# Performance work log

Hardware: AMD Instinct MI355X
Metric: run time of the kernel (lower is better)

The kernel has to match this reference:

```python
import jax, jax.numpy as jnp
import numpy as np

T, B, OBS, H, A = 512, 512, 128, 128, 18


def setup_inputs() -> dict:
    key = jax.random.key(0)
    ks = jax.random.split(key, 8)
    return {
        "hidden": jnp.zeros((B, H), jnp.float32),
        "obs": jax.random.normal(ks[0], (T, B, OBS), jnp.float32),
        "dones": jax.random.bernoulli(ks[1], 0.01, (T, B)),
        # embedding Dense (orthogonal-ish scale sqrt(2))
        "W_emb": jax.random.normal(ks[2], (OBS, H), jnp.float32) * (np.sqrt(2.0) / np.sqrt(OBS)).astype(np.float32),
        "b_emb": jnp.zeros((H,), jnp.float32),
        # GRUCell params: input path Wi/bi cover gates [r | z | n]; hidden path Wh (no bias for r,z), bhn for n
        "Wi": jax.random.normal(ks[3], (H, 3 * H), jnp.float32) / np.float32(np.sqrt(H)),
        "bi": jnp.zeros((3 * H,), jnp.float32),
        "Wh": jax.random.normal(ks[4], (H, 3 * H), jnp.float32) / np.float32(np.sqrt(H)),
        "bhn": jnp.zeros((H,), jnp.float32),
        # output Dense to action_dim
        "W_out": jax.random.normal(ks[5], (H, A), jnp.float32) / np.float32(np.sqrt(H)),
        "b_out": jnp.zeros((A,), jnp.float32),
    }


def reference(hidden, obs, dones, W_emb, b_emb, Wi, bi, Wh, bhn, W_out, b_out):
    # Dense embed + relu: [T, B, OBS] -> [T, B, H]
    emb = jax.nn.relu(obs @ W_emb + b_emb)
    # precompute input-path gate pre-activations for all steps: [T, B, 3H]
    gi = emb @ Wi + bi

    def step(h, xs):
        gi_t, reset = xs  # [B, 3H], [B]
        # reset-masked carry: initialize_carry gives zeros
        h = jnp.where(reset[:, None], jnp.zeros_like(h), h)
        gh = h @ Wh  # [B, 3H]
        r = jax.nn.sigmoid(gi_t[:, :H] + gh[:, :H])
        z = jax.nn.sigmoid(gi_t[:, H:2 * H] + gh[:, H:2 * H])
        n = jnp.tanh(gi_t[:, 2 * H:] + r * (gh[:, 2 * H:] + bhn))
        h_new = (1.0 - z) * n + z * h
        return h_new, h_new

    h_final, ys = jax.lax.scan(step, hidden, (gi, dones))  # ys: [T, B, H]
    q_vals = ys @ W_out + b_out  # [T, B, A]
    return (h_final, q_vals)
```

## Files before the change

### kernel.cpp

```cpp
#include <hip/hip_runtime.h>

#define T_DIM 512
#define B_DIM 512
#define OBS_DIM 128
#define H_DIM 128
#define A_DIM 18
#define G3 384
#define LDSS 136

#define SC_R (-1.44269504088896f)
#define SC_N (2.88539008177793f)

typedef _Float16 v8h __attribute__((ext_vector_type(8)));
typedef _Float16 v4h __attribute__((ext_vector_type(4)));
typedef float v4f __attribute__((ext_vector_type(4)));

#define EXP2F(x) __builtin_amdgcn_exp2f(x)
#define RCPF(x)  __builtin_amdgcn_rcpf(x)

#define BAR() asm volatile("s_waitcnt lgkmcnt(0)\n\ts_barrier" ::: "memory")

__global__ __launch_bounds__(512) void k1_embed_gi(
    const float* __restrict__ obs,
    const float* __restrict__ W_emb,
    const float* __restrict__ b_emb,
    const float* __restrict__ Wi,
    const float* __restrict__ bi,
    _Float16* __restrict__ gRZ,
    _Float16* __restrict__ gN)
{
    __shared__ __align__(16) _Float16 obs_lds[64 * LDSS];
    __shared__ __align__(16) _Float16 emb_lds[64 * LDSS];
    const int tid  = threadIdx.x;
    const int cg   = tid >> 6;
    const int lane = tid & 63;
    const int n16  = lane & 15;
    const int quad = lane >> 4;

    v8h fe[4];
    v8h fi[3][4];
#pragma unroll
    for (int kt = 0; kt < 4; ++kt)
#pragma unroll
        for (int j = 0; j < 8; ++j) {
            const int k = kt * 32 + quad * 8 + j;
            fe[kt][j] = (_Float16)W_emb[k * H_DIM + cg * 16 + n16];
        }
#pragma unroll
    for (int g = 0; g < 3; ++g) {
        const float sc = (g == 2) ? SC_N : SC_R;
#pragma unroll
        for (int kt = 0; kt < 4; ++kt)
#pragma unroll
            for (int j = 0; j < 8; ++j) {
                const int k = kt * 32 + quad * 8 + j;
                fi[g][kt][j] = (_Float16)(Wi[k * G3 + g * H_DIM + cg * 16 + n16] * sc);
            }
    }
    float bemb[4], bir[4], biz[4], bin_[4];
#pragma unroll
    for (int r = 0; r < 4; ++r) {
        const int col = cg * 16 + quad * 4 + r;
        bemb[r] = b_emb[col];
        bir[r]  = bi[col] * SC_R;
        biz[r]  = bi[H_DIM + col] * SC_R;
        bin_[r] = bi[2 * H_DIM + col] * SC_N;
    }

    const int srow = tid >> 3;
    const int sk   = (tid & 7) * 16;
    const int base = blockIdx.x * 16;

    {
        const float* op = obs + (size_t)(base * 64 + srow) * OBS_DIM + sk;
#pragma unroll
        for (int q = 0; q < 4; ++q) {
            const float4 a = *(const float4*)(op + q * 4);
            v4h pa = { (_Float16)a.x, (_Float16)a.y, (_Float16)a.z, (_Float16)a.w };
            *(v4h*)&obs_lds[srow * LDSS + sk + q * 4] = pa;
        }
    }
    __syncthreads();

    for (int i = 0; i < 16; ++i) {
        const int row0 = (base + i) * 64;
        const int ni = (i + 1 < 16) ? i + 1 : i;
        const float* opn = obs + (size_t)((base + ni) * 64 + srow) * OBS_DIM + sk;
        float4 nv[4];
#pragma unroll
        for (int q = 0; q < 4; ++q) nv[q] = *(const float4*)(opn + q * 4);

#pragma unroll
        for (int rt = 0; rt < 4; ++rt) {
            v8h bo[4];
#pragma unroll
            for (int kt = 0; kt < 4; ++kt)
                bo[kt] = *(const v8h*)&obs_lds[(rt * 16 + n16) * LDSS + kt * 32 + quad * 8];
            v4f ea = {0.f, 0.f, 0.f, 0.f};
#pragma unroll
            for (int kt = 0; kt < 4; ++kt)
                ea = __builtin_amdgcn_mfma_f32_16x16x32_f16(fe[kt], bo[kt], ea, 0, 0, 0);
            v4h e;
#pragma unroll
            for (int r = 0; r < 4; ++r) e[r] = (_Float16)fmaxf(ea[r] + bemb[r], 0.f);
            *(v4h*)&emb_lds[(rt * 16 + n16) * LDSS + cg * 16 + quad * 4] = e;
        }
        BAR();
#pragma unroll
        for (int rt = 0; rt < 4; ++rt) {
            v8h be[4];
#pragma unroll
            for (int kt = 0; kt < 4; ++kt)
                be[kt] = *(const v8h*)&emb_lds[(rt * 16 + n16) * LDSS + kt * 32 + quad * 8];
            v4f ar = {0.f,0.f,0.f,0.f}, az = {0.f,0.f,0.f,0.f}, an = {0.f,0.f,0.f,0.f};
#pragma unroll
            for (int kt = 0; kt < 4; ++kt) {
                ar = __builtin_amdgcn_mfma_f32_16x16x32_f16(fi[0][kt], be[kt], ar, 0, 0, 0);
                az = __builtin_amdgcn_mfma_f32_16x16x32_f16(fi[1][kt], be[kt], az, 0, 0, 0);
                an = __builtin_amdgcn_mfma_f32_16x16x32_f16(fi[2][kt], be[kt], an, 0, 0, 0);
            }
            const int R = row0 + rt * 16 + n16;
            v8h rz;
#pragma unroll
            for (int r = 0; r < 4; ++r) {
                rz[r]     = (_Float16)(ar[r] + bir[r]);
                rz[4 + r] = (_Float16)(az[r] + biz[r]);
            }
            *(v8h*)&gRZ[(size_t)R * 256 + cg * 32 + quad * 8] = rz;
            v4h nn;
#pragma unroll
            for (int r = 0; r < 4; ++r) nn[r] = (_Float16)(an[r] + bin_[r]);
            *(v4h*)&gN[(size_t)R * 128 + cg * 16 + quad * 4] = nn;
        }
#pragma unroll
        for (int q = 0; q < 4; ++q) {
            v4h pa = { (_Float16)nv[q].x, (_Float16)nv[q].y, (_Float16)nv[q].z, (_Float16)nv[q].w };
            *(v4h*)&obs_lds[srow * LDSS + sk + q * 4] = pa;
        }
        BAR();
    }
}

__global__ __launch_bounds__(512) void k2_recurrence(
    const float* __restrict__ hidden,
    const unsigned char* __restrict__ dones_raw,
    const _Float16* __restrict__ gRZ,
    _Float16* __restrict__ gN,
    const float* __restrict__ Wh,
    const float* __restrict__ bhn,
    float* __restrict__ out)
{
    __shared__ __align__(16) _Float16 h_lds[2][16 * LDSS];
    __shared__ __align__(16) unsigned char d_lds[(T_DIM + 1) * 16];
    __shared__ int byte_mode;
    const int tid  = threadIdx.x;
    const int w    = tid >> 6;
    const int lane = tid & 63;
    const int n16  = lane & 15;
    const int quad = lane >> 4;
    const int c16  = w * 16 + quad * 4;
    const int B0   = blockIdx.x * 16;

    if (tid == 0) byte_mode = 0;
    __syncthreads();
    {
        int hit = 0;
        for (int i = tid; i < 4096; i += 512)
            if ((i & 3) != 0 && dones_raw[i] == 1) hit = 1;
        if (hit) byte_mode = 1;
    }
    __syncthreads();
    const bool bm = (byte_mode != 0);

    {
        if (bm) {
            const int4 v = *(const int4*)(dones_raw + (size_t)tid * B_DIM + B0);
            *(int4*)&d_lds[tid * 16] = v;
        } else {
            const int* di = (const int*)dones_raw;
            const int* pp = di + (size_t)tid * B_DIM + B0;
            int4 wv; unsigned char* wb = (unsigned char*)&wv;
#pragma unroll
            for (int j = 0; j < 16; ++j) wb[j] = (unsigned char)(pp[j] != 0);
            *(int4*)&d_lds[tid * 16] = wv;
        }
        if (tid == 0) { int4 z = {0,0,0,0}; *(int4*)&d_lds[T_DIM * 16] = z; }
    }

    v8h fh[3][4];
#pragma unroll
    for (int g = 0; g < 3; ++g) {
        const float sc = (g == 2) ? SC_N : SC_R;
#pragma unroll
        for (int kt = 0; kt < 4; ++kt)
#pragma unroll
            for (int j = 0; j < 8; ++j) {
                const int k = kt * 32 + quad * 8 + j;
                fh[g][kt][j] = (_Float16)(Wh[k * G3 + g * H_DIM + w * 16 + n16] * sc);
            }
    }
    float bhnr[4];
#pragma unroll
    for (int r = 0; r < 4; ++r) bhnr[r] = bhn[c16 + r] * SC_N;

    __syncthreads();

    const bool d0 = d_lds[n16] != 0;
    float hu[4];
#pragma unroll
    for (int r = 0; r < 4; ++r) {
        const float hv = hidden[(size_t)(B0 + n16) * H_DIM + c16 + r];
        hu[r] = d0 ? 0.f : hv;
    }
    {
        v4h hw = { (_Float16)hu[0], (_Float16)hu[1], (_Float16)hu[2], (_Float16)hu[3] };
        *(v4h*)&h_lds[0][n16 * LDSS + c16] = hw;
    }

    const size_t RZT = (size_t)B_DIM * 256;
    const size_t NT  = (size_t)B_DIM * 128;
    const _Float16* rzp = gRZ + (size_t)(B0 + n16) * 256 + w * 32 + quad * 8;
    _Float16*       np  = gN  + (size_t)(B0 + n16) * 128 + c16;

    v8h s8_0 = *(const v8h*)(rzp);
    v4h s4_0 = *(const v4h*)(np);
    v8h s8_1 = *(const v8h*)(rzp + RZT);
    v4h s4_1 = *(const v4h*)(np + NT);
    const _Float16* pf8 = rzp + 2 * RZT;
    const _Float16* pf4 = np + 2 * NT;
    _Float16* yp = np;
    const unsigned char* dp = &d_lds[16 + n16];
    __syncthreads();

    auto STEP = [&](int t, v8h& s8, v4h& s4, const _Float16* hin, _Float16* hout)
        __attribute__((always_inline)) -> void {
        const v8h gC8 = *(const v8h*)pf8;
        const v4h gC4 = *(const v4h*)pf4;
        const unsigned char dnx = *dp;

        v8h bh[4];
#pragma unroll
        for (int kt = 0; kt < 4; ++kt)
            bh[kt] = *(const v8h*)&hin[n16 * LDSS + kt * 32 + quad * 8];

        v4f ga0 = {0.f,0.f,0.f,0.f}, ga1 = {0.f,0.f,0.f,0.f}, ga2 = {0.f,0.f,0.f,0.f};
#pragma unroll
        for (int kt = 0; kt < 4; ++kt) {
            ga0 = __builtin_amdgcn_mfma_f32_16x16x32_f16(fh[0][kt], bh[kt], ga0, 0, 0, 0);
            ga1 = __builtin_amdgcn_mfma_f32_16x16x32_f16(fh[1][kt], bh[kt], ga1, 0, 0, 0);
            ga2 = __builtin_amdgcn_mfma_f32_16x16x32_f16(fh[2][kt], bh[kt], ga2, 0, 0, 0);
        }

        float hn[4];
#pragma unroll
        for (int r = 0; r < 4; ++r) {
            const float er = EXP2F((float)s8[r] + ga0[r]);
            const float rg = RCPF(1.f + er);
            const float sn = fmaf(rg, ga2[r] + bhnr[r], (float)s4[r]);
            const float en = EXP2F(sn);
            const float ez = EXP2F((float)s8[4 + r] + ga1[r]);
            const float enp = en + 1.f;
            const float num = fmaf(hu[r], enp, (en - 1.f) * ez);
            const float den = enp * (1.f + ez);
            hn[r] = num * RCPF(den);
        }

        v4h yv = { (_Float16)hn[0], (_Float16)hn[1], (_Float16)hn[2], (_Float16)hn[3] };
        *(v4h*)yp = yv;

        const bool dn = dnx != 0;
        v4h hz = { (_Float16)0.f, (_Float16)0.f, (_Float16)0.f, (_Float16)0.f };
        v4h hv = dn ? hz : yv;
#pragma unroll
        for (int r = 0; r < 4; ++r) hu[r] = dn ? 0.f : hn[r];
        *(v4h*)&hout[n16 * LDSS + c16] = hv;

        s8 = gC8; s4 = gC4;
        const size_t adv = (t < 509) ? 1 : 0;
        pf8 += adv * RZT; pf4 += adv * NT;
        yp += NT; dp += 16;
        BAR();
    };

    for (int t = 0; t < T_DIM; t += 2) {
        STEP(t,     s8_0, s4_0, h_lds[0], h_lds[1]);
        STEP(t + 1, s8_1, s4_1, h_lds[1], h_lds[0]);
    }

#pragma unroll
    for (int r = 0; r < 4; ++r)
        out[(size_t)(B0 + n16) * H_DIM + c16 + r] = hu[r];
}

__global__ __launch_bounds__(256) void k3_qout(
    const _Float16* __restrict__ ys,
    const float* __restrict__ W_out,
    const float* __restrict__ b_out,
    float* __restrict__ qout)
{
    const int tid  = threadIdx.x;
    const int wv   = tid >> 6;
    const int lane = tid & 63;
    const int n16  = lane & 15;
    const int quad = lane >> 4;
    const int R0   = blockIdx.x * 64 + wv * 16;

    v8h fo[2][4];
#pragma unroll
    for (int ct = 0; ct < 2; ++ct)
#pragma unroll
        for (int kt = 0; kt < 4; ++kt)
#pragma unroll
            for (int j = 0; j < 8; ++j) {
                const int k = kt * 32 + quad * 8 + j;
                const int col = ct * 16 + n16;
                fo[ct][kt][j] = (col < A_DIM) ? (_Float16)W_out[k * A_DIM + col] : (_Float16)0.f;
            }
    float bq0[4], bq1[4];
#pragma unroll
    for (int r = 0; r < 4; ++r) {
        const int c0 = quad * 4 + r;
        const int c1 = 16 + quad * 4 + r;
        bq0[r] = b_out[c0];
        bq1[r] = (c1 < A_DIM) ? b_out[c1] : 0.f;
    }

    v8h by[4];
#pragma unroll
    for (int kt = 0; kt < 4; ++kt)
        by[kt] = *(const v8h*)(ys + (size_t)(R0 + n16) * 128 + kt * 32 + quad * 8);
    v4f q0 = {0.f,0.f,0.f,0.f}, q1 = {0.f,0.f,0.f,0.f};
#pragma unroll
    for (int kt = 0; kt < 4; ++kt) {
        q0 = __builtin_amdgcn_mfma_f32_16x16x32_f16(fo[0][kt], by[kt], q0, 0, 0, 0);
        q1 = __builtin_amdgcn_mfma_f32_16x16x32_f16(fo[1][kt], by[kt], q1, 0, 0, 0);
    }
    float* qp = qout + (size_t)(R0 + n16) * A_DIM;
#pragma unroll
    for (int r = 0; r < 4; ++r) qp[quad * 4 + r] = q0[r] + bq0[r];
    if (quad == 0) {
#pragma unroll
        for (int r = 0; r < 2; ++r) qp[16 + r] = q1[r] + bq1[r];
    }
}

extern "C" void kernel_launch(void* const* d_in, const int* in_sizes, int n_in,
                              void* d_out, int out_size, void* d_ws, size_t ws_size,
                              hipStream_t stream) {
    const float* hidden = (const float*)d_in[0];
    const float* obs    = (const float*)d_in[1];
    const unsigned char* dones = (const unsigned char*)d_in[2];
    const float* W_emb  = (const float*)d_in[3];
    const float* b_emb  = (const float*)d_in[4];
    const float* Wi     = (const float*)d_in[5];
    const float* bi     = (const float*)d_in[6];
    const float* Wh     = (const float*)d_in[7];
    const float* bhn    = (const float*)d_in[8];
    const float* W_out  = (const float*)d_in[9];
    const float* b_out  = (const float*)d_in[10];
    float* out = (float*)d_out;

    _Float16* gRZ = (_Float16*)d_ws;
    _Float16* gN  = gRZ + (size_t)T_DIM * B_DIM * 256;

    hipLaunchKernelGGL(k1_embed_gi, dim3(256), dim3(512), 0, stream,
                       obs, W_emb, b_emb, Wi, bi, gRZ, gN);
    hipLaunchKernelGGL(k2_recurrence, dim3(32), dim3(512), 0, stream,
                       hidden, dones, gRZ, gN, Wh, bhn, out);
    hipLaunchKernelGGL(k3_qout, dim3(4096), dim3(256), 0, stream,
                       gN, W_out, b_out, out + (size_t)B_DIM * H_DIM);
}
```

Baseline: 698.9 us.

## Process two 16-row batch tiles per recurrence block, halving grid size

The GRU recurrence kernel now has each block handle 32 batch rows as two 16-row tiles instead of 16, so the Wh fragments held in registers are reused across two MFMA chains per step. The grid drops from 32 to 16 blocks. The aim is to give each wave independent MFMA and transcendental work to overlap within the serial per-step chain, and to pay one barrier per step for twice as many rows. It also folds bhn into the n-gate accumulator init and switches to byte-offset addressing. The cost is more register pressure, a longer critical path per step, and only 16 CUs in use.

New measurement: 1.021 ms. +46.1%, slower.

```diff
diff --git a/kernel.cpp b/kernel.cpp
--- a/kernel.cpp
+++ b/kernel.cpp
@@ -150,8 +150,8 @@
     const float* __restrict__ bhn,
     float* __restrict__ out)
 {
-    __shared__ __align__(16) _Float16 h_lds[2][16 * LDSS];
-    __shared__ __align__(16) unsigned char d_lds[(T_DIM + 1) * 16];
+    __shared__ __align__(16) _Float16 h_lds[2][32 * LDSS];
+    __shared__ __align__(16) unsigned char d_lds[(T_DIM + 1) * 32];
     __shared__ int byte_mode;
     const int tid  = threadIdx.x;
     const int w    = tid >> 6;
@@ -159,7 +159,7 @@
     const int n16  = lane & 15;
     const int quad = lane >> 4;
     const int c16  = w * 16 + quad * 4;
-    const int B0   = blockIdx.x * 16;
+    const int B0   = blockIdx.x * 32;
 
     if (tid == 0) byte_mode = 0;
     __syncthreads();
@@ -173,18 +173,20 @@
     const bool bm = (byte_mode != 0);
 
     {
-        if (bm) {
-            const int4 v = *(const int4*)(dones_raw + (size_t)tid * B_DIM + B0);
-            *(int4*)&d_lds[tid * 16] = v;
-        } else {
-            const int* di = (const int*)dones_raw;
-            const int* pp = di + (size_t)tid * B_DIM + B0;
-            int4 wv; unsigned char* wb = (unsigned char*)&wv;
-#pragma unroll
-            for (int j = 0; j < 16; ++j) wb[j] = (unsigned char)(pp[j] != 0);
-            *(int4*)&d_lds[tid * 16] = wv;
-        }
-        if (tid == 0) { int4 z = {0,0,0,0}; *(int4*)&d_lds[T_DIM * 16] = z; }
+        for (int i = tid; i < T_DIM * 2; i += 512) {
+            const int t = i >> 1, half = i & 1;
+            if (bm) {
+                const int4 v = *(const int4*)(dones_raw + (size_t)t * B_DIM + B0 + half * 16);
+                *(int4*)&d_lds[t * 32 + half * 16] = v;
+            } else {
+                const int* pp = (const int*)dones_raw + (size_t)t * B_DIM + B0 + half * 16;
+                int4 wv; unsigned char* wb = (unsigned char*)&wv;
+#pragma unroll
+                for (int j = 0; j < 16; ++j) wb[j] = (unsigned char)(pp[j] != 0);
+                *(int4*)&d_lds[t * 32 + half * 16] = wv;
+            }
+        }
+        if (tid < 2) { int4 z = {0,0,0,0}; *(int4*)&d_lds[T_DIM * 32 + tid * 16] = z; }
     }
 
     v8h fh[3][4];
@@ -199,86 +201,115 @@
                 fh[g][kt][j] = (_Float16)(Wh[k * G3 + g * H_DIM + w * 16 + n16] * sc);
             }
     }
-    float bhnr[4];
-#pragma unroll
-    for (int r = 0; r < 4; ++r) bhnr[r] = bhn[c16 + r] * SC_N;
+    const v4f bhn_c = { bhn[c16] * SC_N, bhn[c16 + 1] * SC_N,
+                        bhn[c16 + 2] * SC_N, bhn[c16 + 3] * SC_N };
 
     __syncthreads();
 
-    const bool d0 = d_lds[n16] != 0;
-    float hu[4];
-#pragma unroll
-    for (int r = 0; r < 4; ++r) {
-        const float hv = hidden[(size_t)(B0 + n16) * H_DIM + c16 + r];
-        hu[r] = d0 ? 0.f : hv;
-    }
-    {
-        v4h hw = { (_Float16)hu[0], (_Float16)hu[1], (_Float16)hu[2], (_Float16)hu[3] };
-        *(v4h*)&h_lds[0][n16 * LDSS + c16] = hw;
-    }
-
-    const size_t RZT = (size_t)B_DIM * 256;
-    const size_t NT  = (size_t)B_DIM * 128;
-    const _Float16* rzp = gRZ + (size_t)(B0 + n16) * 256 + w * 32 + quad * 8;
-    _Float16*       np  = gN  + (size_t)(B0 + n16) * 128 + c16;
-
-    v8h s8_0 = *(const v8h*)(rzp);
-    v4h s4_0 = *(const v4h*)(np);
-    v8h s8_1 = *(const v8h*)(rzp + RZT);
-    v4h s4_1 = *(const v4h*)(np + NT);
-    const _Float16* pf8 = rzp + 2 * RZT;
-    const _Float16* pf4 = np + 2 * NT;
-    _Float16* yp = np;
-    const unsigned char* dp = &d_lds[16 + n16];
+    float hu[2][4];
+#pragma unroll
+    for (int rt = 0; rt < 2; ++rt) {
+        const bool d0 = d_lds[rt * 16 + n16] != 0;
+#pragma unroll
+        for (int r = 0; r < 4; ++r) {
+            const float hv = hidden[(size_t)(B0 + rt * 16 + n16) * H_DIM + c16 + r];
+            hu[rt][r] = d0 ? 0.f : hv;
+        }
+        v4h hw = { (_Float16)hu[rt][0], (_Float16)hu[rt][1],
+                   (_Float16)hu[rt][2], (_Float16)hu[rt][3] };
+        *(v4h*)&h_lds[0][(rt * 16 + n16) * LDSS + c16] = hw;
+    }
+
+    const int RZB = B_DIM * 256 * 2;
+    const int NB  = B_DIM * 128 * 2;
+    int rzo[2], no_[2];
+#pragma unroll
+    for (int rt = 0; rt < 2; ++rt) {
+        rzo[rt] = ((B0 + rt * 16 + n16) * 256 + w * 32 + quad * 8) * 2;
+        no_[rt] = ((B0 + rt * 16 + n16) * 128 + c16) * 2;
+    }
+    const char* gRZc = (const char*)gRZ;
+    char*       gNc  = (char*)gN;
+
+    v8h s8_0[2], s8_1[2]; v4h s4_0[2], s4_1[2];
+#pragma unroll
+    for (int rt = 0; rt < 2; ++rt) {
+        s8_0[rt] = *(const v8h*)(gRZc + rzo[rt]);
+        s8_1[rt] = *(const v8h*)(gRZc + RZB + rzo[rt]);
+        s4_0[rt] = *(const v4h*)(gNc + no_[rt]);
+        s4_1[rt] = *(const v4h*)(gNc + NB + no_[rt]);
+    }
+    const char* rzb = gRZc + (size_t)2 * RZB;
+    const char* nb  = gNc  + (size_t)2 * NB;
+    char*       yb  = gNc;
+    int dpo = 32 + n16;
     __syncthreads();
 
-    auto STEP = [&](int t, v8h& s8, v4h& s4, const _Float16* hin, _Float16* hout)
+    auto STEP = [&](int t, v8h (&s8)[2], v4h (&s4)[2],
+                    const _Float16* __restrict__ hin, _Float16* __restrict__ hout)
         __attribute__((always_inline)) -> void {
-        const v8h gC8 = *(const v8h*)pf8;
-        const v4h gC4 = *(const v4h*)pf4;
-        const unsigned char dnx = *dp;
-
-        v8h bh[4];
-#pragma unroll
-        for (int kt = 0; kt < 4; ++kt)
-            bh[kt] = *(const v8h*)&hin[n16 * LDSS + kt * 32 + quad * 8];
-
-        v4f ga0 = {0.f,0.f,0.f,0.f}, ga1 = {0.f,0.f,0.f,0.f}, ga2 = {0.f,0.f,0.f,0.f};
-#pragma unroll
-        for (int kt = 0; kt < 4; ++kt) {
-            ga0 = __builtin_amdgcn_mfma_f32_16x16x32_f16(fh[0][kt], bh[kt], ga0, 0, 0, 0);
-            ga1 = __builtin_amdgcn_mfma_f32_16x16x32_f16(fh[1][kt], bh[kt], ga1, 0, 0, 0);
-            ga2 = __builtin_amdgcn_mfma_f32_16x16x32_f16(fh[2][kt], bh[kt], ga2, 0, 0, 0);
-        }
-
-        float hn[4];
-#pragma unroll
-        for (int r = 0; r < 4; ++r) {
-            const float er = EXP2F((float)s8[r] + ga0[r]);
-            const float rg = RCPF(1.f + er);
-            const float sn = fmaf(rg, ga2[r] + bhnr[r], (float)s4[r]);
-            const float en = EXP2F(sn);
-            const float ez = EXP2F((float)s8[4 + r] + ga1[r]);
-            const float enp = en + 1.f;
-            const float num = fmaf(hu[r], enp, (en - 1.f) * ez);
-            const float den = enp * (1.f + ez);
-            hn[r] = num * RCPF(den);
-        }
-
-        v4h yv = { (_Float16)hn[0], (_Float16)hn[1], (_Float16)hn[2], (_Float16)hn[3] };
-        *(v4h*)yp = yv;
-
-        const bool dn = dnx != 0;
-        v4h hz = { (_Float16)0.f, (_Float16)0.f, (_Float16)0.f, (_Float16)0.f };
-        v4h hv = dn ? hz : yv;
-#pragma unroll
-        for (int r = 0; r < 4; ++r) hu[r] = dn ? 0.f : hn[r];
-        *(v4h*)&hout[n16 * LDSS + c16] = hv;
-
-        s8 = gC8; s4 = gC4;
-        const size_t adv = (t < 509) ? 1 : 0;
-        pf8 += adv * RZT; pf4 += adv * NT;
-        yp += NT; dp += 16;
+        v8h gC8[2]; v4h gC4[2]; unsigned char dnx[2];
+#pragma unroll
+        for (int rt = 0; rt < 2; ++rt) gC8[rt] = *(const v8h*)(rzb + rzo[rt]);
+#pragma unroll
+        for (int rt = 0; rt < 2; ++rt) gC4[rt] = *(const v4h*)(nb + no_[rt]);
+#pragma unroll
+        for (int rt = 0; rt < 2; ++rt) dnx[rt] = d_lds[dpo + rt * 16];
+
+        v8h bh[2][4];
+#pragma unroll
+        for (int rt = 0; rt < 2; ++rt)
+#pragma unroll
+            for (int kt = 0; kt < 4; ++kt)
+                bh[rt][kt] = *(const v8h*)&hin[(rt * 16 + n16) * LDSS + kt * 32 + quad * 8];
+
+        v4f ga0[2], ga1[2], ga2[2];
+#pragma unroll
+        for (int rt = 0; rt < 2; ++rt) {
+            ga0[rt] = (v4f){0.f,0.f,0.f,0.f};
+            ga1[rt] = (v4f){0.f,0.f,0.f,0.f};
+            ga2[rt] = bhn_c;
+        }
+#pragma unroll
+        for (int rt = 0; rt < 2; ++rt)
+#pragma unroll
+            for (int kt = 0; kt < 4; ++kt) {
+                ga0[rt] = __builtin_amdgcn_mfma_f32_16x16x32_f16(fh[0][kt], bh[rt][kt], ga0[rt], 0, 0, 0);
+                ga1[rt] = __builtin_amdgcn_mfma_f32_16x16x32_f16(fh[1][kt], bh[rt][kt], ga1[rt], 0, 0, 0);
+                ga2[rt] = __builtin_amdgcn_mfma_f32_16x16x32_f16(fh[2][kt], bh[rt][kt], ga2[rt], 0, 0, 0);
+            }
+
+#pragma unroll
+        for (int rt = 0; rt < 2; ++rt) {
+            float hn[4];
+#pragma unroll
+            for (int r = 0; r < 4; ++r) {
+                const float er  = EXP2F((float)s8[rt][r] + ga0[rt][r]);
+                const float rg  = RCPF(1.f + er);
+                const float sn  = fmaf(rg, ga2[rt][r], (float)s4[rt][r]);
+                const float en  = EXP2F(sn);
+                const float ez  = EXP2F((float)s8[rt][4 + r] + ga1[rt][r]);
+                const float enp = en + 1.f;
+                const float num = fmaf(hu[rt][r], enp, (en - 1.f) * ez);
+                const float den = enp * (1.f + ez);
+                hn[r] = num * RCPF(den);
+            }
+
+            v4h yv = { (_Float16)hn[0], (_Float16)hn[1], (_Float16)hn[2], (_Float16)hn[3] };
+            *(v4h*)(yb + no_[rt]) = yv;
+
+            const bool dn = dnx[rt] != 0;
+            v4h hz = { (_Float16)0.f, (_Float16)0.f, (_Float16)0.f, (_Float16)0.f };
+            v4h hv = dn ? hz : yv;
+#pragma unroll
+            for (int r = 0; r < 4; ++r) hu[rt][r] = dn ? 0.f : hn[r];
+            *(v4h*)&hout[(rt * 16 + n16) * LDSS + c16] = hv;
+
+            s8[rt] = gC8[rt]; s4[rt] = gC4[rt];
+        }
+
+        if (t <= 508) { rzb += RZB; nb += NB; }
+        yb += NB; dpo += 32;
         BAR();
     };
 
@@ -288,8 +319,10 @@
     }
 
 #pragma unroll
-    for (int r = 0; r < 4; ++r)
-        out[(size_t)(B0 + n16) * H_DIM + c16 + r] = hu[r];
+    for (int rt = 0; rt < 2; ++rt)
+#pragma unroll
+        for (int r = 0; r < 4; ++r)
+            out[(size_t)(B0 + rt * 16 + n16) * H_DIM + c16 + r] = hu[rt][r];
 }
 
 __global__ __launch_bounds__(256) void k3_qout(
@@ -365,7 +398,7 @@
 
     hipLaunchKernelGGL(k1_embed_gi, dim3(256), dim3(512), 0, stream,
                        obs, W_emb, b_emb, Wi, bi, gRZ, gN);
-    hipLaunchKernelGGL(k2_recurrence, dim3(32), dim3(512), 0, stream,
+    hipLaunchKernelGGL(k2_recurrence, dim3(16), dim3(512), 0, stream,
                        hidden, dones, gRZ, gN, Wh, bhn, out);
     hipLaunchKernelGGL(k3_qout, dim3(4096), dim3(256), 0, stream,
                        gN, W_out, b_out, out + (size_t)B_DIM * H_DIM);
```
